# Kernel optimization log

Measured on AMD Instinct MI355X. Metric: run time of the kernel, lower is better.

Reference implementation:

```python
import jax, jax.numpy as jnp
import numpy as np
from jax import lax

H = 64  # LSTM units (hard-coded in the module)


def _lstm(x, W, U, b, return_sequences):
    """Keras-style LSTM (inference; recurrent_dropout inactive).
    x: [B, T, F]; W: [F, 4H]; U: [H, 4H]; b: [4H].
    Gate order (Keras): i, f, g(cell), o.
    """
    B = x.shape[0]
    # Precompute input contribution for all timesteps: [T, B, 4H]
    xz = jnp.einsum('btf,fg->tbg', x, W) + b

    def step(carry, z_t):
        h, c = carry
        z = z_t + h @ U  # [B, 4H]
        i = jax.nn.sigmoid(z[:, :H])
        f = jax.nn.sigmoid(z[:, H:2 * H])
        g = jnp.tanh(z[:, 2 * H:3 * H])
        o = jax.nn.sigmoid(z[:, 3 * H:])
        c = f * c + i * g
        h = o * jnp.tanh(c)
        return (h, c), h

    init = (jnp.zeros((B, H), x.dtype), jnp.zeros((B, H), x.dtype))
    (h_last, _), hs = lax.scan(step, init, xz)
    if return_sequences:
        return jnp.transpose(hs, (1, 0, 2))  # [B, T, H]
    return h_last  # [B, H]


def setup_inputs() -> dict:
    key = jax.random.key(0)
    ks = jax.random.split(key, 8)
    B, T, F = 4096, 256, 32
    s_in = 1.0 / np.sqrt(F)
    s_h = 1.0 / np.sqrt(H)
    return {
        'x': jax.random.normal(ks[0], (B, T, F), jnp.float32),
        'W1': jax.random.normal(ks[1], (F, 4 * H), jnp.float32) * s_in,
        'U1': jax.random.normal(ks[2], (H, 4 * H), jnp.float32) * s_h,
        'b1': jnp.zeros((4 * H,), jnp.float32),
        'W2': jax.random.normal(ks[3], (H, 4 * H), jnp.float32) * s_h,
        'U2': jax.random.normal(ks[4], (H, 4 * H), jnp.float32) * s_h,
        'b2': jnp.zeros((4 * H,), jnp.float32),
        'Wd': jax.random.normal(ks[5], (H, H), jnp.float32) * s_h,
        'bd': jnp.zeros((H,), jnp.float32),
        'Wo': jax.random.normal(ks[6], (H, 1), jnp.float32) * s_h,
        'bo': jnp.zeros((1,), jnp.float32),
    }


def reference(x, W1, U1, b1, W2, U2, b2, Wd, bd, Wo, bo):
    h_seq = _lstm(x, W1, U1, b1, return_sequences=True)   # hidden_lstm
    h_last = _lstm(h_seq, W2, U2, b2, return_sequences=False)  # lstm_layer
    d = jax.nn.sigmoid(h_last @ Wd + bd)  # Dense(64, sigmoid)
    return jax.nn.sigmoid(d @ Wo + bo)    # Dense(1, sigmoid) -> [B, 1]
```

## Files before the change

kernel.cpp:

```cpp
#include <hip/hip_runtime.h>


typedef __attribute__((ext_vector_type(8))) short short8;
typedef __attribute__((ext_vector_type(4))) float floatx4;
typedef __attribute__((ext_vector_type(2))) float floatx2;

__device__ __forceinline__ float ex2(float x){ return __builtin_amdgcn_exp2f(x); }
__device__ __forceinline__ float rcp_(float x){ return __builtin_amdgcn_rcpf(x); }
__device__ __forceinline__ float sigm(float x){ return rcp_(1.0f + ex2(-1.44269504f*x)); }
__device__ __forceinline__ unsigned bfbits(float f){
    unsigned u = __builtin_bit_cast(unsigned, f);
    u += 0x7FFFu + ((u >> 16) & 1u);
    return u >> 16;
}
__device__ __forceinline__ short f2bf(float f){ return (short)bfbits(f); }
__device__ __forceinline__ unsigned cvtpk(float lo, float hi){
    unsigned r;
    asm("v_cvt_pk_bf16_f32 %0, %1, %2" : "=v"(r) : "v"(lo), "v"(hi));
    return r;
}
__device__ __forceinline__ void wg_barrier_lds(){
    asm volatile("s_waitcnt lgkmcnt(0)\n\ts_barrier" ::: "memory");
}

#define MFMA_BF16 __builtin_amdgcn_mfma_f32_16x16x32_bf16

__global__ __launch_bounds__(1024, 1)
void lstm2_tz(const float* __restrict__ x,
              const float* __restrict__ W1, const float* __restrict__ U1, const float* __restrict__ b1,
              const float* __restrict__ W2, const float* __restrict__ U2, const float* __restrict__ b2,
              const float* __restrict__ Wd, const float* __restrict__ bd,
              const float* __restrict__ Wo, const float* __restrict__ bo,
              float* __restrict__ out)
{
    __shared__ __align__(16) short h1b[2][16 * 64];
    __shared__ __align__(16) short h2b[2][16 * 64];
    __shared__ __align__(16) short xsb[2][16 * 40];
    __shared__ float psum[4][16];

    const int tid  = threadIdx.x;
    const int w    = tid >> 6;
    const bool isL1 = (w < 8);
    const int wv   = w & 7;
    const int lane = tid & 63;
    const int n    = lane & 15;
    const int q    = lane >> 4;
    const int b0   = blockIdx.x * 16;

    const float LG = 1.44269504f;

    const int ugl = n >> 2;
    const int gA  = n & 3;
    const float sA = (gA == 2) ? (2.0f * LG) : (-LG);

    const int sw   = n & 7;
    const int hro0 = n * 64 + ((q ^ sw) << 3);
    const int hro1 = n * 64 + (((4 + q) ^ sw) << 3);
    const int xro  = n * 40 + q * 8;
    const int hwo  = n * 64 + ((wv ^ sw) << 3) + q * 2;

    short8  Wa[8];
    floatx4 bC[2];
    if (isL1) {
#pragma unroll
        for (int tt = 0; tt < 2; ++tt) {
            const int un   = wv * 8 + ugl * 2 + tt;
            const int ncol = gA * 64 + un;
#pragma unroll
            for (int j = 0; j < 8; ++j) {
                const int k = q * 8 + j;
                Wa[tt * 3 + 0][j] = f2bf(W1[k * 256 + ncol] * sA);
                Wa[tt * 3 + 1][j] = f2bf(U1[k * 256 + ncol] * sA);
                Wa[tt * 3 + 2][j] = f2bf(U1[(32 + k) * 256 + ncol] * sA);
            }
#pragma unroll
            for (int r = 0; r < 4; ++r)
                bC[tt][r] = b1[r * 64 + wv * 8 + q * 2 + tt] * ((r == 2) ? (2.0f * LG) : (-LG));
        }
    } else {
#pragma unroll
        for (int tt = 0; tt < 2; ++tt) {
            const int un   = wv * 8 + ugl * 2 + tt;
            const int ncol = gA * 64 + un;
#pragma unroll
            for (int j = 0; j < 8; ++j) {
                const int k = q * 8 + j;
                Wa[tt * 4 + 0][j] = f2bf(W2[k * 256 + ncol] * sA);
                Wa[tt * 4 + 1][j] = f2bf(W2[(32 + k) * 256 + ncol] * sA);
                Wa[tt * 4 + 2][j] = f2bf(U2[k * 256 + ncol] * sA);
                Wa[tt * 4 + 3][j] = f2bf(U2[(32 + k) * 256 + ncol] * sA);
            }
#pragma unroll
            for (int r = 0; r < 4; ++r)
                bC[tt][r] = b2[r * 64 + wv * 8 + q * 2 + tt] * ((r == 2) ? (2.0f * LG) : (-LG));
        }
    }

    {
        unsigned* p1 = (unsigned*)&h1b[0][0];
        unsigned* p2 = (unsigned*)&h2b[0][0];
        for (int i = tid; i < 1024; i += 1024) { p1[i] = 0u; p2[i] = 0u; }
    }

    const int xr = tid >> 4;
    const int xc = (tid & 15) * 2;
    const float* xrow = x + (size_t)(b0 + xr) * 8192 + xc;
    floatx2 xv0;
    if (tid < 256) {
        floatx2 v = *(const floatx2*)xrow;
        *(unsigned*)&xsb[0][xr * 40 + xc] = cvtpk(v.x, v.y);
        xv0 = *(const floatx2*)(xrow + 32);
    }
    __syncthreads();

    float c[2] = {0, 0};

    for (int u = 0; u <= 256; ++u) {
        const int par = u & 1, pax = par ^ 1;
        if (isL1) {
            if (u < 256) {
                const short* hR = &h1b[pax][0];
                short8 bx  = *(const short8*)&xsb[par][xro];
                short8 bh0 = *(const short8*)&hR[hro0];
                short8 bh1 = *(const short8*)&hR[hro1];
                if (tid < 256 && u < 255) {
                    *(unsigned*)&xsb[pax][xr * 40 + xc] = cvtpk(xv0.x, xv0.y);
                    if (u < 254) xv0 = *(const floatx2*)(xrow + (size_t)(u + 2) * 32);
                }
                float hv[2];
#pragma unroll
                for (int tt = 0; tt < 2; ++tt) {
                    floatx4 z = bC[tt];
                    z = MFMA_BF16(Wa[tt * 3 + 0], bx,  z, 0, 0, 0);
                    z = MFMA_BF16(Wa[tt * 3 + 1], bh0, z, 0, 0, 0);
                    z = MFMA_BF16(Wa[tt * 3 + 2], bh1, z, 0, 0, 0);
                    float iv = rcp_(1.0f + ex2(z[0]));
                    float fv = rcp_(1.0f + ex2(z[1]));
                    float rg = rcp_(1.0f + ex2(z[2]));
                    float ov = rcp_(1.0f + ex2(z[3]));
                    float gp = fmaf(-5.77078016f, rg, 2.88539008f);
                    c[tt] = fmaf(fv, c[tt], iv * gp);
                    float th = fmaf(-2.0f, rcp_(1.0f + ex2(c[tt])), 1.0f);
                    hv[tt] = ov * th;
                }
                *(unsigned*)&h1b[par][hwo] = cvtpk(hv[0], hv[1]);
            }
        } else {
            if (u >= 1) {
                const short* hR = &h1b[pax][0];
                const short* gR = &h2b[par][0];
                short8 bh0 = *(const short8*)&hR[hro0];
                short8 bh1 = *(const short8*)&hR[hro1];
                short8 bg0 = *(const short8*)&gR[hro0];
                short8 bg1 = *(const short8*)&gR[hro1];
                float hv[2];
#pragma unroll
                for (int tt = 0; tt < 2; ++tt) {
                    floatx4 z = bC[tt];
                    z = MFMA_BF16(Wa[tt * 4 + 0], bh0, z, 0, 0, 0);
                    z = MFMA_BF16(Wa[tt * 4 + 1], bh1, z, 0, 0, 0);
                    z = MFMA_BF16(Wa[tt * 4 + 2], bg0, z, 0, 0, 0);
                    z = MFMA_BF16(Wa[tt * 4 + 3], bg1, z, 0, 0, 0);
                    float iv = rcp_(1.0f + ex2(z[0]));
                    float fv = rcp_(1.0f + ex2(z[1]));
                    float rg = rcp_(1.0f + ex2(z[2]));
                    float ov = rcp_(1.0f + ex2(z[3]));
                    float gp = fmaf(-5.77078016f, rg, 2.88539008f);
                    c[tt] = fmaf(fv, c[tt], iv * gp);
                    float th = fmaf(-2.0f, rcp_(1.0f + ex2(c[tt])), 1.0f);
                    hv[tt] = ov * th;
                }
                *(unsigned*)&h2b[pax][hwo] = cvtpk(hv[0], hv[1]);
            }
        }
        wg_barrier_lds();
    }

    if (!isL1 && wv < 4) {
        const int colD = wv * 16 + n;
        short8 wd0, wd1;
#pragma unroll
        for (int j = 0; j < 8; ++j) {
            wd0[j] = f2bf(Wd[(q * 8 + j) * 64 + colD] * (-LG));
            wd1[j] = f2bf(Wd[(32 + q * 8 + j) * 64 + colD] * (-LG));
        }
        short8 hA0 = *(const short8*)&h2b[1][hro0];
        short8 hA1 = *(const short8*)&h2b[1][hro1];
        const float bdv = bd[colD] * (-LG);
        floatx4 dacc = { bdv, bdv, bdv, bdv };
        dacc = MFMA_BF16(hA0, wd0, dacc, 0, 0, 0);
        dacc = MFMA_BF16(hA1, wd1, dacc, 0, 0, 0);
        const float wo = Wo[colD];
#pragma unroll
        for (int r = 0; r < 4; ++r) {
            float p = rcp_(1.0f + ex2(dacc[r])) * wo;
            p += __shfl_xor(p, 1, 64);
            p += __shfl_xor(p, 2, 64);
            p += __shfl_xor(p, 4, 64);
            p += __shfl_xor(p, 8, 64);
            if (n == 0) psum[wv][q * 4 + r] = p;
        }
    }
    __syncthreads();
    if (tid < 16) {
        float s = psum[0][tid] + psum[1][tid] + psum[2][tid] + psum[3][tid] + bo[0];
        out[b0 + tid] = sigm(s);
    }
}

extern "C" void kernel_launch(void* const* d_in, const int* in_sizes, int n_in,
                              void* d_out, int out_size, void* d_ws, size_t ws_size,
                              hipStream_t stream) {
    (void)in_sizes; (void)n_in; (void)d_ws; (void)ws_size; (void)out_size;
    const float* x  = (const float*)d_in[0];
    const float* W1 = (const float*)d_in[1];
    const float* U1 = (const float*)d_in[2];
    const float* b1 = (const float*)d_in[3];
    const float* W2 = (const float*)d_in[4];
    const float* U2 = (const float*)d_in[5];
    const float* b2 = (const float*)d_in[6];
    const float* Wd = (const float*)d_in[7];
    const float* bd = (const float*)d_in[8];
    const float* Wo = (const float*)d_in[9];
    const float* bo = (const float*)d_in[10];
    lstm2_tz<<<dim3(256), dim3(1024), 0, stream>>>(
        x, W1, U1, b1, W2, U2, b2, Wd, bd, Wo, bo, (float*)d_out);
}
```

Baseline: 349.4 us.

## Split LSTM step into two phases so layer-1 MFMA overlaps layer-2 gate math

```diff
diff --git a/kernel.cpp b/kernel.cpp
--- a/kernel.cpp
+++ b/kernel.cpp
@@ -21,6 +21,16 @@
 }
 __device__ __forceinline__ void wg_barrier_lds(){
     asm volatile("s_waitcnt lgkmcnt(0)\n\ts_barrier" ::: "memory");
+}
+__device__ __forceinline__ float gate_update(const floatx4& z, float& c){
+    float iv = rcp_(1.0f + ex2(z[0]));
+    float fv = rcp_(1.0f + ex2(z[1]));
+    float rg = rcp_(1.0f + ex2(z[2]));
+    float ov = rcp_(1.0f + ex2(z[3]));
+    float gp = fmaf(-5.77078016f, rg, 2.88539008f);
+    c = fmaf(fv, c, iv * gp);
+    float th = fmaf(-2.0f, rcp_(1.0f + ex2(c)), 1.0f);
+    return ov * th;
 }
 
 #define MFMA_BF16 __builtin_amdgcn_mfma_f32_16x16x32_bf16
@@ -114,9 +124,11 @@
     __syncthreads();
 
     float c[2] = {0, 0};
-
-    for (int u = 0; u <= 256; ++u) {
+    floatx4 z[2];
+
+    for (int u = 0; u <= 257; ++u) {
         const int par = u & 1, pax = par ^ 1;
+
         if (isL1) {
             if (u < 256) {
                 const short* hR = &h1b[pax][0];
@@ -127,50 +139,47 @@
                     *(unsigned*)&xsb[pax][xr * 40 + xc] = cvtpk(xv0.x, xv0.y);
                     if (u < 254) xv0 = *(const floatx2*)(xrow + (size_t)(u + 2) * 32);
                 }
-                float hv[2];
 #pragma unroll
                 for (int tt = 0; tt < 2; ++tt) {
-                    floatx4 z = bC[tt];
-                    z = MFMA_BF16(Wa[tt * 3 + 0], bx,  z, 0, 0, 0);
-                    z = MFMA_BF16(Wa[tt * 3 + 1], bh0, z, 0, 0, 0);
-                    z = MFMA_BF16(Wa[tt * 3 + 2], bh1, z, 0, 0, 0);
-                    float iv = rcp_(1.0f + ex2(z[0]));
-                    float fv = rcp_(1.0f + ex2(z[1]));
-                    float rg = rcp_(1.0f + ex2(z[2]));
-                    float ov = rcp_(1.0f + ex2(z[3]));
-                    float gp = fmaf(-5.77078016f, rg, 2.88539008f);
-                    c[tt] = fmaf(fv, c[tt], iv * gp);
-                    float th = fmaf(-2.0f, rcp_(1.0f + ex2(c[tt])), 1.0f);
-                    hv[tt] = ov * th;
+                    floatx4 zz = bC[tt];
+                    zz = MFMA_BF16(Wa[tt * 3 + 0], bx,  zz, 0, 0, 0);
+                    zz = MFMA_BF16(Wa[tt * 3 + 1], bh0, zz, 0, 0, 0);
+                    zz = MFMA_BF16(Wa[tt * 3 + 2], bh1, zz, 0, 0, 0);
+                    z[tt] = zz;
                 }
-                *(unsigned*)&h1b[par][hwo] = cvtpk(hv[0], hv[1]);
             }
         } else {
-            if (u >= 1) {
+            if (u >= 2) {
+                float hv0 = gate_update(z[0], c[0]);
+                float hv1 = gate_update(z[1], c[1]);
+                *(unsigned*)&h2b[par][hwo] = cvtpk(hv0, hv1);
+            }
+        }
+        wg_barrier_lds();
+
+        if (isL1) {
+            if (u < 256) {
+                float hv0 = gate_update(z[0], c[0]);
+                float hv1 = gate_update(z[1], c[1]);
+                *(unsigned*)&h1b[par][hwo] = cvtpk(hv0, hv1);
+            }
+        } else {
+            if (u >= 1 && u <= 256) {
                 const short* hR = &h1b[pax][0];
                 const short* gR = &h2b[par][0];
                 short8 bh0 = *(const short8*)&hR[hro0];
                 short8 bh1 = *(const short8*)&hR[hro1];
                 short8 bg0 = *(const short8*)&gR[hro0];
                 short8 bg1 = *(const short8*)&gR[hro1];
-                float hv[2];
 #pragma unroll
                 for (int tt = 0; tt < 2; ++tt) {
-                    floatx4 z = bC[tt];
-                    z = MFMA_BF16(Wa[tt * 4 + 0], bh0, z, 0, 0, 0);
-                    z = MFMA_BF16(Wa[tt * 4 + 1], bh1, z, 0, 0, 0);
-                    z = MFMA_BF16(Wa[tt * 4 + 2], bg0, z, 0, 0, 0);
-                    z = MFMA_BF16(Wa[tt * 4 + 3], bg1, z, 0, 0, 0);
-                    float iv = rcp_(1.0f + ex2(z[0]));
-                    float fv = rcp_(1.0f + ex2(z[1]));
-                    float rg = rcp_(1.0f + ex2(z[2]));
-                    float ov = rcp_(1.0f + ex2(z[3]));
-                    float gp = fmaf(-5.77078016f, rg, 2.88539008f);
-                    c[tt] = fmaf(fv, c[tt], iv * gp);
-                    float th = fmaf(-2.0f, rcp_(1.0f + ex2(c[tt])), 1.0f);
-                    hv[tt] = ov * th;
+                    floatx4 zz = bC[tt];
+                    zz = MFMA_BF16(Wa[tt * 4 + 0], bh0, zz, 0, 0, 0);
+                    zz = MFMA_BF16(Wa[tt * 4 + 1], bh1, zz, 0, 0, 0);
+                    zz = MFMA_BF16(Wa[tt * 4 + 2], bg0, zz, 0, 0, 0);
+                    zz = MFMA_BF16(Wa[tt * 4 + 3], bg1, zz, 0, 0, 0);
+                    z[tt] = zz;
                 }
-                *(unsigned*)&h2b[pax][hwo] = cvtpk(hv[0], hv[1]);
             }
         }
         wg_barrier_lds();
```

Measured after the change: 366.7 us. 4.9% more time.
